# Performance work log

Hardware: AMD Instinct MI355X
Metric: run time of the kernel (lower is better)

Reference implementation:

```python
import jax, jax.numpy as jnp
import numpy as np

# dims
B, N, D = 256, 77, 768     # batch, CLIP tokens, token dim
K, Dn, H = 16, 768, 8      # nodes, node dim, heads
HID, L = 512, 2            # edge-MLP hidden, num GNN layers


def setup_inputs() -> dict:
    key = jax.random.key(0)
    ks = jax.random.split(key, 12)
    g = lambda k, shape, s=0.02: (jax.random.normal(k, shape, jnp.float32) * s)
    return {
        "w": jax.random.normal(ks[0], (B, N, D), jnp.float32),
        "token_mask": jax.random.randint(ks[1], (B, N), 0, 2).astype(jnp.int32),
        "node_queries": g(ks[2], (1, K, Dn)),
        "Wq": g(ks[3], (Dn, Dn)), "bq": jnp.zeros((Dn,), jnp.float32),
        "Wk": g(ks[4], (D, Dn)),  "bk": jnp.zeros((Dn,), jnp.float32),
        "Wv": g(ks[5], (D, Dn)),  "bv": jnp.zeros((Dn,), jnp.float32),
        "We1": g(ks[6], (2 * Dn, HID)), "be1": jnp.zeros((HID,), jnp.float32),
        "We2": g(ks[7], (HID, 1)),      "be2": jnp.zeros((1,), jnp.float32),
        "fuse_gate": jnp.float32(0.0),
        "Wg": g(ks[8], (L, Dn, Dn)), "bg": jnp.zeros((L, Dn), jnp.float32),
    }


def _edge_logits(V, We1, be1, We2, be2):
    # edge_mlp(cat[Vi, Vj]) without materializing [B,K,K,2Dn]:
    # split first linear into the Vi-half and Vj-half of its weight.
    hi = V @ We1[:Dn]   # [B,K,HID]
    hj = V @ We1[Dn:]   # [B,K,HID]
    h = jax.nn.relu(hi[:, :, None, :] + hj[:, None, :, :] + be1)  # [B,K,K,HID]
    return jnp.einsum('bijh,h->bij', h, We2[:, 0]) + be2[0]       # [B,K,K]


def _forward(w, node_queries, Wq, bq, Wk, bk, Wv, bv,
             We1, be1, We2, be2, fuse_gate, Wg, bg, token_mask):
    q = jnp.broadcast_to(node_queries, (B, K, Dn))
    Q = q @ Wq + bq        # [B,K,Dn]
    Kt = w @ Wk + bk       # [B,N,Dn]
    Vt = w @ Wv + bv       # [B,N,Dn]
    # per-head dot products summed over heads == full Dn dot product
    scale = (Dn // H) ** -0.5
    scores = jnp.einsum('bkd,bnd->bkn', Q, Kt) * scale  # [B,K,N]
    pad = (token_mask == 0)[:, None, :]                 # [B,1,N]
    scores = jnp.where(pad, jnp.finfo(scores.dtype).min, scores)
    # softmax over K per token (transpose to [B,N,K])
    S = jax.nn.softmax(jnp.swapaxes(scores, 1, 2), axis=-1)  # [B,N,K]
    V = jnp.einsum('bnk,bnd->bkd', S, Vt)                    # [B,K,Dn]
    gate = jax.nn.sigmoid(fuse_gate)
    V = (1.0 - gate) * V + gate * q
    # pre-GNN edge logits, then relational GNN refinement
    E = _edge_logits(V, We1, be1, We2, be2)
    A = jax.nn.softmax(E, axis=-1)  # [B,K,K], fixed across layers
    for l in range(L):
        msg = jnp.einsum('bij,bjd->bid', A, V @ Wg[l] + bg[l])
        V = V + jax.nn.relu(msg)
    # post-GNN edge logits
    E = _edge_logits(V, We1, be1, We2, be2)
    return S, V, E


def reference(w, token_mask, node_queries, Wq, bq, Wk, bk, Wv, bv,
              We1, be1, We2, be2, fuse_gate, Wg, bg):
    return _forward(w, node_queries, Wq, bq, Wk, bk, Wv, bv,
                    We1, be1, We2, be2, fuse_gate, Wg, bg, token_mask)
```

## Files before the change

kernel.cpp:

```cpp
#include <hip/hip_runtime.h>

typedef unsigned short u16;
typedef __attribute__((ext_vector_type(8))) short short8;
typedef __attribute__((ext_vector_type(4))) float f32x4;

#define DEV static __device__ __forceinline__

DEV float bf2f(u16 u) { return __uint_as_float(((unsigned)u) << 16); }
DEV u16 f2bf(float f) {
  unsigned u = __float_as_uint(f);
  return (u16)((u + 0x7fffu + ((u >> 16) & 1u)) >> 16);
}

DEV void cp16(void* lds, const void* g) {
  __builtin_amdgcn_global_load_lds(
      (const __attribute__((address_space(1))) unsigned int*)g,
      (__attribute__((address_space(3))) unsigned int*)lds, 16, 0, 0);
}

DEV int xcd_swz() {
  int bid = blockIdx.x;
  int cpx = gridDim.x >> 3;
  return (bid & 7) * cpx + (bid >> 3);
}


__global__ __launch_bounds__(256) void tcast_all(const float* __restrict__ Wv,
                                                 const float* __restrict__ We1,
                                                 const float* __restrict__ Wg,
                                                 u16* __restrict__ WvT,
                                                 u16* __restrict__ We1T,
                                                 u16* __restrict__ WgT) {
  __shared__ float tile[32][33];
  const float* src; u16* dst; int C;
  switch (blockIdx.z) {
    case 0: src = Wv;           dst = WvT;           C = 768; break;
    case 1: src = We1;          dst = We1T;          C = 512; break;
    case 2: src = We1 + 393216; dst = We1T + 393216; C = 512; break;
    case 3: src = Wg;           dst = WgT;           C = 768; break;
    default: src = Wg + 589824; dst = WgT + 589824;  C = 768; break;
  }
  int r0 = blockIdx.y * 32, c0 = blockIdx.x * 32;
  if (c0 >= C) return;
  int tr = threadIdx.x >> 5, tc = threadIdx.x & 31;
#pragma unroll
  for (int rr = 0; rr < 4; ++rr)
    tile[tr + rr * 8][tc] = src[(size_t)(r0 + tr + rr * 8) * C + c0 + tc];
  __syncthreads();
#pragma unroll
  for (int rr = 0; rr < 4; ++rr)
    dst[(size_t)(c0 + tr + rr * 8) * 768 + r0 + tc] = f2bf(tile[tc][tr + rr * 8]);
}

__global__ __launch_bounds__(256) void q_part(const float* __restrict__ nq,
                                              const float* __restrict__ Wq,
                                              float* __restrict__ Qpart) {
  int gid = blockIdx.x * 256 + threadIdx.x;
  int s = blockIdx.y;
  int k = gid / 768, d = gid % 768;
  const float* nr = nq + k * 768 + s * 96;
  const float* wp = Wq + (size_t)(s * 96) * 768 + d;
  float s0 = 0.f, s1 = 0.f, s2 = 0.f, s3 = 0.f;
#pragma unroll
  for (int c = 0; c < 96; c += 4) {
    s0 += nr[c + 0] * wp[(size_t)(c + 0) * 768];
    s1 += nr[c + 1] * wp[(size_t)(c + 1) * 768];
    s2 += nr[c + 2] * wp[(size_t)(c + 2) * 768];
    s3 += nr[c + 3] * wp[(size_t)(c + 3) * 768];
  }
  Qpart[(size_t)s * 12288 + gid] = (s0 + s1) + (s2 + s3);
}

__global__ __launch_bounds__(256) void q_reduce(const float* __restrict__ Qpart,
                                                const float* __restrict__ bq,
                                                float* __restrict__ Qf) {
  int gid = blockIdx.x * 256 + threadIdx.x;
  int d = gid % 768;
  float s = bq[d];
#pragma unroll
  for (int i = 0; i < 8; ++i) s += Qpart[(size_t)i * 12288 + gid];
  Qf[gid] = s;
}

__global__ __launch_bounds__(256) void pt_kernel(const float* __restrict__ Qf,
                                                 const float* __restrict__ Wk,
                                                 const float* __restrict__ bk,
                                                 u16* __restrict__ PT16,
                                                 float* __restrict__ qb) {
  int t = threadIdx.x;
  if (blockIdx.x == 48) {
    int k = t >> 4, j = t & 15;
    const float* q = Qf + k * 768 + j * 48;
    const float* bp = bk + j * 48;
    float s = 0.f;
#pragma unroll
    for (int d = 0; d < 48; d += 4) {
      f32x4 qv = *(const f32x4*)&q[d];
      f32x4 bv4 = *(const f32x4*)&bp[d];
      s += qv[0] * bv4[0] + qv[1] * bv4[1] + qv[2] * bv4[2] + qv[3] * bv4[3];
    }
#pragma unroll
    for (int off = 1; off < 16; off <<= 1) s += __shfl_xor(s, off);
    if (j == 0) qb[k] = s;
    return;
  }
  int gid = blockIdx.x * 256 + t;
  int c = gid >> 4, k = gid & 15;
  const float* wr = Wk + (size_t)c * 768;
  const float* q = Qf + k * 768;
  float s = 0.f;
  for (int d = 0; d < 768; d += 4) {
    f32x4 wv = *(const f32x4*)&wr[d];
    f32x4 qv = *(const f32x4*)&q[d];
    s += wv[0] * qv[0] + wv[1] * qv[1] + wv[2] * qv[2] + wv[3] * qv[3];
  }
  PT16[k * 768 + c] = f2bf(s);
}

__global__ __launch_bounds__(256) void score2(const float* __restrict__ w,
                                              const u16* __restrict__ PT16,
                                              const float* __restrict__ qb,
                                              const int* __restrict__ mask,
                                              float* __restrict__ Sout) {
  __shared__ u16 Ps[16 * 776];
  int t = threadIdx.x, wave = t >> 6, lane = t & 63, l16 = lane & 15, quad = lane >> 4;
  int m0 = blockIdx.x * 64;
#pragma unroll
  for (int r = 0; r < 6; ++r) {
    int idx = t + 256 * r;
    int row = idx / 96, c8 = idx % 96;
    *(short8*)&Ps[row * 776 + c8 * 8] = *(const short8*)&PT16[row * 768 + c8 * 8];
  }
  __syncthreads();
  int row = m0 + wave * 16 + l16;
  const float* ap = w + (size_t)row * 768 + quad * 8;
  f32x4 acc = {0.f, 0.f, 0.f, 0.f};
#pragma unroll
  for (int it = 0; it < 24; ++it) {
    f32x4 a0 = *(const f32x4*)(ap + it * 32);
    f32x4 a1 = *(const f32x4*)(ap + it * 32 + 4);
    short8 fa;
#pragma unroll
    for (int e = 0; e < 4; ++e) { fa[e] = (short)f2bf(a0[e]); fa[e + 4] = (short)f2bf(a1[e]); }
    short8 fb = *(const short8*)&Ps[l16 * 776 + it * 32 + quad * 8];
    acc = __builtin_amdgcn_mfma_f32_16x16x32_bf16(fa, fb, acc, 0, 0, 0);
  }
  float qv = qb[l16];
  const float scale = 0.1020620726159658f;
#pragma unroll
  for (int r = 0; r < 4; ++r) {
    int orow = m0 + wave * 16 + quad * 4 + r;
    float s = (acc[r] + qv) * scale;
    if (mask[orow] == 0) s = -3.402823466e38f;
    float mx = s;
#pragma unroll
    for (int off = 1; off < 16; off <<= 1) mx = fmaxf(mx, __shfl_xor(mx, off));
    float e = __expf(s - mx);
    float sm = e;
#pragma unroll
    for (int off = 1; off < 16; off <<= 1) sm += __shfl_xor(sm, off);
    Sout[(size_t)orow * 16 + l16] = e / sm;
  }
}

__global__ __launch_bounds__(256) void u_kernel(const float* __restrict__ Sg,
                                                const float* __restrict__ w,
                                                u16* __restrict__ U16,
                                                float* __restrict__ sk) {
  __shared__ float Ss[1232];
  int b = blockIdx.x, t = threadIdx.x;
  int d = blockIdx.y * 256 + t;
#pragma unroll
  for (int r = 0; r < 5; ++r) {
    int idx = t + 256 * r;
    if (idx < 1232) Ss[idx] = Sg[(size_t)b * 1232 + idx];
  }
  __syncthreads();
  float a[16];
#pragma unroll
  for (int k = 0; k < 16; ++k) a[k] = 0.f;
  const float* wp = w + (size_t)b * 59136;
  for (int n = 0; n < 77; ++n) {
    float g = wp[(size_t)n * 768 + d];
    const float* sr = &Ss[n * 16];
#pragma unroll
    for (int k = 0; k < 16; ++k) a[k] += sr[k] * g;
  }
#pragma unroll
  for (int k = 0; k < 16; ++k)
    U16[(size_t)b * 12288 + (size_t)k * 768 + d] = f2bf(a[k]);
  if (blockIdx.y == 0 && t < 16) {
    float s = 0.f;
    for (int n = 0; n < 77; ++n) s += Ss[n * 16 + t];
    sk[b * 16 + t] = s;
  }
}

#define STAGE3(KOFF, BI)                          \
  do {                                            \
    cp16(AsW + (BI) * 2048, Ap + (KOFF));         \
    cp16(BsW1 + (BI) * 4096, Bp1 + (KOFF));       \
    cp16(BsW2 + (BI) * 4096, Bp2 + (KOFF));       \
  } while (0)

__global__ __launch_bounds__(256) void vgemm(const u16* __restrict__ A,
                                             const u16* __restrict__ BT,
                                             const float* __restrict__ skp,
                                             const float* __restrict__ bv,
                                             const float* __restrict__ nq,
                                             const float* __restrict__ gatep,
                                             float* __restrict__ V32,
                                             u16* __restrict__ V16) {
  __shared__ u16 As[3 * 64 * 32];
  __shared__ u16 Bs[3 * 128 * 32];
  int swz = xcd_swz();
  int mi = swz / 6, ni = swz % 6;
  int m0 = mi * 64, n0 = ni * 128;
  int t = threadIdx.x;
  int wave = t >> 6, lane = t & 63, l16 = lane & 15, quad = lane >> 4;
  int ra = wave * 16 + (lane >> 2);
  int rb1 = wave * 32 + (lane >> 2);
  int rb2 = rb1 + 16;
  int cslot = lane & 3;
  int cga = (cslot ^ ((ra >> 1) & 3)) * 8;
  int cgb1 = (cslot ^ ((rb1 >> 1) & 3)) * 8;
  int cgb2 = (cslot ^ ((rb2 >> 1) & 3)) * 8;

  const u16* Ap = A + (size_t)(m0 + ra) * 768 + cga;
  const u16* Bp1 = BT + (size_t)(n0 + rb1) * 768 + cgb1;
  const u16* Bp2 = BT + (size_t)(n0 + rb2) * 768 + cgb2;
  u16* AsW = &As[(wave * 16) * 32];
  u16* BsW1 = &Bs[(wave * 32) * 32];
  u16* BsW2 = &Bs[(wave * 32 + 16) * 32];

  f32x4 zero4 = {0.f, 0.f, 0.f, 0.f};
  f32x4 acc[4][2];
#pragma unroll
  for (int i = 0; i < 4; ++i) { acc[i][0] = zero4; acc[i][1] = zero4; }

  STAGE3(0, 0); STAGE3(32, 1); STAGE3(64, 2);

  int bi = 0;
  for (int k0 = 0; k0 < 768; k0 += 32) {
    int rem = (768 - 32 - k0) >> 5;
    if (rem >= 2)      asm volatile("s_waitcnt vmcnt(6)" ::: "memory");
    else if (rem == 1) asm volatile("s_waitcnt vmcnt(3)" ::: "memory");
    else               asm volatile("s_waitcnt vmcnt(0)" ::: "memory");
    asm volatile("s_barrier" ::: "memory");
    const u16* Ab = &As[bi * 2048];
    const u16* Bb = &Bs[bi * 4096];
    short8 fa[4], fb[2];
#pragma unroll
    for (int i = 0; i < 4; ++i) {
      int R = i * 16 + l16;
      fa[i] = *(const short8*)&Ab[R * 32 + (quad ^ ((R >> 1) & 3)) * 8];
    }
#pragma unroll
    for (int j = 0; j < 2; ++j) {
      int R = wave * 32 + j * 16 + l16;
      fb[j] = *(const short8*)&Bb[R * 32 + (quad ^ ((R >> 1) & 3)) * 8];
    }
#pragma unroll
    for (int i = 0; i < 4; ++i)
#pragma unroll
      for (int j = 0; j < 2; ++j)
        acc[i][j] = __builtin_amdgcn_mfma_f32_16x16x32_bf16(fa[i], fb[j], acc[i][j], 0, 0, 0);
    asm volatile("s_barrier" ::: "memory");
    if (k0 + 96 < 768) STAGE3(k0 + 96, bi);
    bi = bi + 1; if (bi == 3) bi = 0;
  }

  float gv = gatep[0];
  float g = 1.f / (1.f + __expf(-gv)), og = 1.f - g;
  int narr[2]; float bvj[2];
#pragma unroll
  for (int j = 0; j < 2; ++j) {
    narr[j] = n0 + wave * 32 + j * 16 + l16;
    bvj[j] = bv[narr[j]];
  }
#pragma unroll
  for (int i = 0; i < 4; ++i)
#pragma unroll
    for (int r = 0; r < 4; ++r) {
      int m = m0 + i * 16 + quad * 4 + r;
      float skv = skp[m];
      size_t mrow = (size_t)m * 768;
      const float* nqr = nq + (m & 15) * 768;
#pragma unroll
      for (int j = 0; j < 2; ++j) {
        float val = acc[i][j][r] + skv * bvj[j];
        float v = og * val + g * nqr[narr[j]];
        V32[mrow + narr[j]] = v;
        V16[mrow + narr[j]] = f2bf(v);
      }
    }
}

__global__ __launch_bounds__(256) void gemm16s(const u16* __restrict__ A,
                                               const u16* __restrict__ BT0,
                                               const float* __restrict__ bias0,
                                               u16* __restrict__ C0, int N0, int ntA,
                                               const u16* __restrict__ BT1,
                                               const float* __restrict__ bias1,
                                               u16* __restrict__ C1, int N1, int ntB,
                                               int K) {
  __shared__ u16 As[3 * 64 * 32];
  __shared__ u16 Bs[3 * 128 * 32];
  int nt = ntA + ntB;
  int swz = xcd_swz();
  int mi = swz / nt, ni = swz % nt;
  const u16* BT; const float* bias; u16* C; int N, n0;
  if (ni < ntA) { BT = BT0; bias = bias0; C = C0; N = N0; n0 = ni * 128; }
  else          { BT = BT1; bias = bias1; C = C1; N = N1; n0 = (ni - ntA) * 128; }
  int m0 = mi * 64;
  int t = threadIdx.x;
  int wave = t >> 6, lane = t & 63, l16 = lane & 15, quad = lane >> 4;
  int ra = wave * 16 + (lane >> 2);
  int rb1 = wave * 32 + (lane >> 2);
  int rb2 = rb1 + 16;
  int cslot = lane & 3;
  int cga = (cslot ^ ((ra >> 1) & 3)) * 8;
  int cgb1 = (cslot ^ ((rb1 >> 1) & 3)) * 8;
  int cgb2 = (cslot ^ ((rb2 >> 1) & 3)) * 8;

  const u16* Ap = A + (size_t)(m0 + ra) * K + cga;
  const u16* Bp1 = BT + (size_t)(n0 + rb1) * K + cgb1;
  const u16* Bp2 = BT + (size_t)(n0 + rb2) * K + cgb2;
  u16* AsW = &As[(wave * 16) * 32];
  u16* BsW1 = &Bs[(wave * 32) * 32];
  u16* BsW2 = &Bs[(wave * 32 + 16) * 32];

  f32x4 zero4 = {0.f, 0.f, 0.f, 0.f};
  f32x4 acc[4][2];
#pragma unroll
  for (int i = 0; i < 4; ++i) { acc[i][0] = zero4; acc[i][1] = zero4; }

  STAGE3(0, 0); STAGE3(32, 1); STAGE3(64, 2);

  int bi = 0;
  for (int k0 = 0; k0 < K; k0 += 32) {
    int rem = (K - 32 - k0) >> 5;
    if (rem >= 2)      asm volatile("s_waitcnt vmcnt(6)" ::: "memory");
    else if (rem == 1) asm volatile("s_waitcnt vmcnt(3)" ::: "memory");
    else               asm volatile("s_waitcnt vmcnt(0)" ::: "memory");
    asm volatile("s_barrier" ::: "memory");
    const u16* Ab = &As[bi * 2048];
    const u16* Bb = &Bs[bi * 4096];
    short8 fa[4], fb[2];
#pragma unroll
    for (int i = 0; i < 4; ++i) {
      int R = i * 16 + l16;
      fa[i] = *(const short8*)&Ab[R * 32 + (quad ^ ((R >> 1) & 3)) * 8];
    }
#pragma unroll
    for (int j = 0; j < 2; ++j) {
      int R = wave * 32 + j * 16 + l16;
      fb[j] = *(const short8*)&Bb[R * 32 + (quad ^ ((R >> 1) & 3)) * 8];
    }
#pragma unroll
    for (int i = 0; i < 4; ++i)
#pragma unroll
      for (int j = 0; j < 2; ++j)
        acc[i][j] = __builtin_amdgcn_mfma_f32_16x16x32_bf16(fa[i], fb[j], acc[i][j], 0, 0, 0);
    asm volatile("s_barrier" ::: "memory");
    if (k0 + 96 < K) STAGE3(k0 + 96, bi);
    bi = bi + 1; if (bi == 3) bi = 0;
  }

  int narr[2]; float bvj[2];
#pragma unroll
  for (int j = 0; j < 2; ++j) {
    narr[j] = n0 + wave * 32 + j * 16 + l16;
    bvj[j] = bias ? bias[narr[j]] : 0.f;
  }
#pragma unroll
  for (int i = 0; i < 4; ++i)
#pragma unroll
    for (int r = 0; r < 4; ++r) {
      size_t mrow = (size_t)(m0 + i * 16 + quad * 4 + r) * N;
#pragma unroll
      for (int j = 0; j < 2; ++j)
        C[mrow + narr[j]] = f2bf(acc[i][j][r] + bvj[j]);
    }
}

__global__ __launch_bounds__(256) void edge_kernel(const u16* __restrict__ HIJ,
                                                   const float* __restrict__ be1,
                                                   const float* __restrict__ We2,
                                                   const float* __restrict__ be2v,
                                                   float* __restrict__ Aout,
                                                   float* __restrict__ Eout) {
  __shared__ float hiS[8 * 516];
  __shared__ float hjS[16 * 516];
  __shared__ float be1s[512];
  __shared__ float w2s[512];
  int b = blockIdx.x, ih = blockIdx.y, t = threadIdx.x;
  be1s[t] = be1[t]; be1s[t + 256] = be1[t + 256];
  w2s[t] = We2[t];  w2s[t + 256] = We2[t + 256];

#pragma unroll
  for (int r = 0; r < 6; ++r) {
    int idx = t + 256 * r;
    const u16* src;
    float* dst;
    if (idx < 512) {
      int row = idx >> 6, c8 = idx & 63;
      src = &HIJ[(size_t)(b * 16 + ih * 8 + row) * 1024 + c8 * 8];
      dst = &hiS[row * 516 + c8 * 8];
    } else {
      int k = idx - 512;
      int row = k >> 6, c8 = k & 63;
      src = &HIJ[(size_t)(b * 16 + row) * 1024 + 512 + c8 * 8];
      dst = &hjS[row * 516 + c8 * 8];
    }
    short8 hv = *(const short8*)src;
    f32x4 l0, l1;
#pragma unroll
    for (int ee = 0; ee < 4; ++ee) { l0[ee] = bf2f((u16)hv[ee]); l1[ee] = bf2f((u16)hv[ee + 4]); }
    *(f32x4*)dst = l0;
    *(f32x4*)(dst + 4) = l1;
  }
  __syncthreads();

  int i_loc = t >> 5, j = (t >> 1) & 15, hh = t & 1;
  const float* hi = &hiS[i_loc * 516 + hh * 256];
  const float* hj = &hjS[j * 516 + hh * 256];
  const float* b1 = &be1s[hh * 256];
  const float* w2 = &w2s[hh * 256];
  float e = 0.f;
#pragma unroll 2
  for (int h4 = 0; h4 < 64; ++h4) {
    f32x4 hv = *(const f32x4*)&hi[h4 * 4];
    f32x4 jv = *(const f32x4*)&hj[h4 * 4];
    f32x4 bv = *(const f32x4*)&b1[h4 * 4];
    f32x4 wv = *(const f32x4*)&w2[h4 * 4];
#pragma unroll
    for (int ee = 0; ee < 4; ++ee)
      e += fmaxf(hv[ee] + jv[ee] + bv[ee], 0.f) * wv[ee];
  }
  e += __shfl_xor(e, 1);
  e += be2v[0];

  int pair = (ih * 8 + i_loc) * 16 + j;
  if (Aout) {
    float mx = e;
#pragma unroll
    for (int off = 2; off < 32; off <<= 1) mx = fmaxf(mx, __shfl_xor(mx, off));
    float ex = __expf(e - mx);
    float sm = ex;
#pragma unroll
    for (int off = 2; off < 32; off <<= 1) sm += __shfl_xor(sm, off);
    if (hh == 0) Aout[(size_t)b * 256 + pair] = ex / sm;
  }
  if (Eout && hh == 0) Eout[(size_t)b * 256 + pair] = e;
}

__global__ __launch_bounds__(256) void combine_kernel(const float* __restrict__ Aws,
                                                      const u16* __restrict__ G,
                                                      float* __restrict__ V32,
                                                      u16* __restrict__ V16,
                                                      float* __restrict__ Vout) {
  __shared__ float Gs[16 * 260];
  __shared__ float As[256];
  int b = blockIdx.x, yc = blockIdx.y, t = threadIdx.x;
#pragma unroll
  for (int r = 0; r < 2; ++r) {
    int idx = t + 256 * r;
    int row = idx >> 5, c8 = idx & 31;
    short8 gv8 = *(const short8*)&G[(size_t)(b * 16 + row) * 768 + yc * 256 + c8 * 8];
    f32x4 l0, l1;
#pragma unroll
    for (int ee = 0; ee < 4; ++ee) { l0[ee] = bf2f((u16)gv8[ee]); l1[ee] = bf2f((u16)gv8[ee + 4]); }
    *(f32x4*)&Gs[row * 260 + c8 * 8] = l0;
    *(f32x4*)&Gs[row * 260 + c8 * 8 + 4] = l1;
  }
  As[t] = Aws[(size_t)b * 256 + t];
  __syncthreads();
  int d = yc * 256 + t;
  float gv[16];
#pragma unroll
  for (int j = 0; j < 16; ++j) gv[j] = Gs[j * 260 + t];
#pragma unroll
  for (int i = 0; i < 16; ++i) {
    float msg = 0.f;
#pragma unroll
    for (int j = 0; j < 16; ++j) msg += As[i * 16 + j] * gv[j];
    size_t idx = (size_t)b * 12288 + (size_t)i * 768 + d;
    float v = V32[idx] + fmaxf(msg, 0.f);
    V32[idx] = v;
    V16[idx] = f2bf(v);
    if (Vout) Vout[idx] = v;
  }
}

extern "C" void kernel_launch(void* const* d_in, const int* in_sizes, int n_in,
                              void* d_out, int out_size, void* d_ws, size_t ws_size,
                              hipStream_t stream) {
  const float* w    = (const float*)d_in[0];
  const int*   mask = (const int*)d_in[1];
  const float* nq   = (const float*)d_in[2];
  const float* Wq   = (const float*)d_in[3];
  const float* bq   = (const float*)d_in[4];
  const float* Wk   = (const float*)d_in[5];
  const float* bk   = (const float*)d_in[6];
  const float* Wv   = (const float*)d_in[7];
  const float* bv   = (const float*)d_in[8];
  const float* We1  = (const float*)d_in[9];
  const float* be1  = (const float*)d_in[10];
  const float* We2  = (const float*)d_in[11];
  const float* be2  = (const float*)d_in[12];
  const float* gate = (const float*)d_in[13];
  const float* Wg   = (const float*)d_in[14];
  const float* bg   = (const float*)d_in[15];

  float* ws    = (float*)d_ws;
  float* V32   = ws;
  float* Aws   = V32 + 3145728;
  float* Qpart = Aws + 65536;
  float* Qf    = Qpart + 98304;
  float* qb    = Qf + 12288;
  float* sk    = qb + 16;
  u16* PT16    = (u16*)(sk + 4096);
  u16* WvT     = PT16 + 12288;
  u16* We1T    = WvT + 589824;
  u16* WgT     = We1T + 786432;
  u16* V16     = WgT + 1179648;
  u16* U16     = V16 + 3145728;
  u16* HIJ     = U16 + 3145728;
  u16* Gws     = HIJ + 4194304;

  float* out  = (float*)d_out;
  float* Sout = out;
  float* Vout = out + 315392;
  float* Eout = out + 315392 + 3145728;

  dim3 blk(256);

  tcast_all<<<dim3(24, 24, 5), blk, 0, stream>>>(Wv, We1, Wg, WvT, We1T, WgT);
  q_part<<<dim3(48, 8), blk, 0, stream>>>(nq, Wq, Qpart);
  q_reduce<<<48, blk, 0, stream>>>(Qpart, bq, Qf);
  pt_kernel<<<49, blk, 0, stream>>>(Qf, Wk, bk, PT16, qb);

  score2<<<308, blk, 0, stream>>>(w, PT16, qb, mask, Sout);

  u_kernel<<<dim3(256, 3), blk, 0, stream>>>(Sout, w, U16, sk);
  vgemm<<<384, blk, 0, stream>>>(U16, WvT, sk, bv, nq, gate, V32, V16);

  gemm16s<<<896, blk, 0, stream>>>(V16, We1T, nullptr, HIJ, 1024, 8,
                                   WgT, bg, Gws, 768, 6, 768);
  edge_kernel<<<dim3(256, 2), blk, 0, stream>>>(HIJ, be1, We2, be2, Aws, (float*)nullptr);
  combine_kernel<<<dim3(256, 3), blk, 0, stream>>>(Aws, Gws, V32, V16, (float*)nullptr);

  gemm16s<<<384, blk, 0, stream>>>(V16, WgT + 589824, bg + 768, Gws, 768, 6,
                                   WgT + 589824, bg + 768, Gws, 768, 0, 768);
  combine_kernel<<<dim3(256, 3), blk, 0, stream>>>(Aws, Gws, V32, V16, Vout);

  gemm16s<<<512, blk, 0, stream>>>(V16, We1T, nullptr, HIJ, 1024, 8,
                                   We1T, nullptr, HIJ, 1024, 0, 768);
  edge_kernel<<<dim3(256, 2), blk, 0, stream>>>(HIJ, be1, We2, be2, (float*)nullptr, Eout);
}
```

Measured before the change: 302.3 us.

## Add 128x128 bf16 MFMA GEMM, merge Q kernels, skip redundant V32 store

Adds a gemm128 kernel that uses 128x128 output tiles, double-buffered LDS fed by global_load_lds, and 16x16x32 bf16 MFMA. It replaces the first fused We1/Wg GEMM launch (448 blocks instead of 896), raising operand reuse per block at the cost of fewer blocks per CU. It also merges the split-K q_part/q_reduce pair into one kernel, which drops a launch but lengthens the serial K loop. In the final combine it writes only Vout rather than both V32 and Vout, removing a redundant store.

After: 316.2 us. 4.6% more time.

```diff
diff --git a/kernel.cpp b/kernel.cpp
--- a/kernel.cpp
+++ b/kernel.cpp
@@ -52,34 +52,23 @@
     dst[(size_t)(c0 + tr + rr * 8) * 768 + r0 + tc] = f2bf(tile[tc][tr + rr * 8]);
 }
 
-__global__ __launch_bounds__(256) void q_part(const float* __restrict__ nq,
-                                              const float* __restrict__ Wq,
-                                              float* __restrict__ Qpart) {
+__global__ __launch_bounds__(256) void q_kernel(const float* __restrict__ nq,
+                                                const float* __restrict__ Wq,
+                                                const float* __restrict__ bq,
+                                                float* __restrict__ Qf) {
   int gid = blockIdx.x * 256 + threadIdx.x;
-  int s = blockIdx.y;
   int k = gid / 768, d = gid % 768;
-  const float* nr = nq + k * 768 + s * 96;
-  const float* wp = Wq + (size_t)(s * 96) * 768 + d;
+  const float* nr = nq + k * 768;
+  const float* wp = Wq + d;
   float s0 = 0.f, s1 = 0.f, s2 = 0.f, s3 = 0.f;
-#pragma unroll
-  for (int c = 0; c < 96; c += 4) {
+#pragma unroll 4
+  for (int c = 0; c < 768; c += 4) {
     s0 += nr[c + 0] * wp[(size_t)(c + 0) * 768];
     s1 += nr[c + 1] * wp[(size_t)(c + 1) * 768];
     s2 += nr[c + 2] * wp[(size_t)(c + 2) * 768];
     s3 += nr[c + 3] * wp[(size_t)(c + 3) * 768];
   }
-  Qpart[(size_t)s * 12288 + gid] = (s0 + s1) + (s2 + s3);
-}
-
-__global__ __launch_bounds__(256) void q_reduce(const float* __restrict__ Qpart,
-                                                const float* __restrict__ bq,
-                                                float* __restrict__ Qf) {
-  int gid = blockIdx.x * 256 + threadIdx.x;
-  int d = gid % 768;
-  float s = bq[d];
-#pragma unroll
-  for (int i = 0; i < 8; ++i) s += Qpart[(size_t)i * 12288 + gid];
-  Qf[gid] = s;
+  Qf[gid] = (s0 + s1) + (s2 + s3) + bq[d];
 }
 
 __global__ __launch_bounds__(256) void pt_kernel(const float* __restrict__ Qf,
@@ -384,6 +373,99 @@
     }
 }
 
+#define STG128(BI, KOFF)                                    \
+  do {                                                      \
+    cp16(&As[(BI) * 4096 + (wave * 32) * 32],      Ap1 + (KOFF)); \
+    cp16(&As[(BI) * 4096 + (wave * 32 + 16) * 32], Ap2 + (KOFF)); \
+    cp16(&Bs[(BI) * 4096 + (wave * 32) * 32],      Bp1 + (KOFF)); \
+    cp16(&Bs[(BI) * 4096 + (wave * 32 + 16) * 32], Bp2 + (KOFF)); \
+  } while (0)
+
+__global__ __launch_bounds__(256) void gemm128(const u16* __restrict__ A,
+                                               const u16* __restrict__ BT0,
+                                               const float* __restrict__ bias0,
+                                               u16* __restrict__ C0, int N0, int ntA,
+                                               const u16* __restrict__ BT1,
+                                               const float* __restrict__ bias1,
+                                               u16* __restrict__ C1, int N1, int ntB,
+                                               int K) {
+  __shared__ u16 As[2 * 128 * 32];
+  __shared__ u16 Bs[2 * 128 * 32];
+  int nt = ntA + ntB;
+  int swz = xcd_swz();
+  int mi = swz / nt, ni = swz % nt;
+  const u16* BT; const float* bias; u16* C; int N, n0;
+  if (ni < ntA) { BT = BT0; bias = bias0; C = C0; N = N0; n0 = ni * 128; }
+  else          { BT = BT1; bias = bias1; C = C1; N = N1; n0 = (ni - ntA) * 128; }
+  int m0 = mi * 128;
+  int t = threadIdx.x;
+  int wave = t >> 6, lane = t & 63, l16 = lane & 15, quad = lane >> 4;
+  int wrow = (wave >> 1) * 64, wcol = (wave & 1) * 64;
+  int r1 = wave * 32 + (lane >> 2);
+  int r2 = r1 + 16;
+  int cslot = lane & 3;
+  int cg1 = (cslot ^ ((r1 >> 1) & 3)) * 8;
+  int cg2 = (cslot ^ ((r2 >> 1) & 3)) * 8;
+
+  const u16* Ap1 = A + (size_t)(m0 + r1) * K + cg1;
+  const u16* Ap2 = A + (size_t)(m0 + r2) * K + cg2;
+  const u16* Bp1 = BT + (size_t)(n0 + r1) * K + cg1;
+  const u16* Bp2 = BT + (size_t)(n0 + r2) * K + cg2;
+
+  f32x4 zero4 = {0.f, 0.f, 0.f, 0.f};
+  f32x4 acc[4][4];
+#pragma unroll
+  for (int i = 0; i < 4; ++i)
+#pragma unroll
+    for (int j = 0; j < 4; ++j) acc[i][j] = zero4;
+
+  STG128(0, 0); STG128(1, 32);
+
+  int cur = 0;
+  for (int k0 = 0; k0 < K; k0 += 32) {
+    if (k0 + 32 < K) asm volatile("s_waitcnt vmcnt(4)" ::: "memory");
+    else             asm volatile("s_waitcnt vmcnt(0)" ::: "memory");
+    asm volatile("s_barrier" ::: "memory");
+    const u16* Ab = &As[cur * 4096];
+    const u16* Bb = &Bs[cur * 4096];
+    short8 fa[4], fb[4];
+#pragma unroll
+    for (int i = 0; i < 4; ++i) {
+      int R = wrow + i * 16 + l16;
+      fa[i] = *(const short8*)&Ab[R * 32 + (quad ^ ((R >> 1) & 3)) * 8];
+    }
+#pragma unroll
+    for (int j = 0; j < 4; ++j) {
+      int R = wcol + j * 16 + l16;
+      fb[j] = *(const short8*)&Bb[R * 32 + (quad ^ ((R >> 1) & 3)) * 8];
+    }
+#pragma unroll
+    for (int i = 0; i < 4; ++i)
+#pragma unroll
+      for (int j = 0; j < 4; ++j)
+        acc[i][j] = __builtin_amdgcn_mfma_f32_16x16x32_bf16(fa[i], fb[j], acc[i][j], 0, 0, 0);
+    asm volatile("s_barrier" ::: "memory");
+    if (k0 + 64 < K) STG128(cur, k0 + 64);
+    cur ^= 1;
+  }
+
+  int narr[4]; float bvj[4];
+#pragma unroll
+  for (int j = 0; j < 4; ++j) {
+    narr[j] = n0 + wcol + j * 16 + l16;
+    bvj[j] = bias ? bias[narr[j]] : 0.f;
+  }
+#pragma unroll
+  for (int i = 0; i < 4; ++i)
+#pragma unroll
+    for (int r = 0; r < 4; ++r) {
+      size_t mrow = (size_t)(m0 + wrow + i * 16 + quad * 4 + r) * N;
+#pragma unroll
+      for (int j = 0; j < 4; ++j)
+        C[mrow + narr[j]] = f2bf(acc[i][j][r] + bvj[j]);
+    }
+}
+
 __global__ __launch_bounds__(256) void edge_kernel(const u16* __restrict__ HIJ,
                                                    const float* __restrict__ be1,
                                                    const float* __restrict__ We2,
@@ -487,9 +569,9 @@
     for (int j = 0; j < 16; ++j) msg += As[i * 16 + j] * gv[j];
     size_t idx = (size_t)b * 12288 + (size_t)i * 768 + d;
     float v = V32[idx] + fmaxf(msg, 0.f);
-    V32[idx] = v;
+    if (Vout) { Vout[idx] = v; }
+    else      { V32[idx] = v; }
     V16[idx] = f2bf(v);
-    if (Vout) Vout[idx] = v;
   }
 }
 
@@ -516,8 +598,7 @@
   float* ws    = (float*)d_ws;
   float* V32   = ws;
   float* Aws   = V32 + 3145728;
-  float* Qpart = Aws + 65536;
-  float* Qf    = Qpart + 98304;
+  float* Qf    = Aws + 65536;
   float* qb    = Qf + 12288;
   float* sk    = qb + 16;
   u16* PT16    = (u16*)(sk + 4096);
@@ -537,8 +618,7 @@
   dim3 blk(256);
 
   tcast_all<<<dim3(24, 24, 5), blk, 0, stream>>>(Wv, We1, Wg, WvT, We1T, WgT);
-  q_part<<<dim3(48, 8), blk, 0, stream>>>(nq, Wq, Qpart);
-  q_reduce<<<48, blk, 0, stream>>>(Qpart, bq, Qf);
+  q_kernel<<<48, blk, 0, stream>>>(nq, Wq, bq, Qf);
   pt_kernel<<<49, blk, 0, stream>>>(Qf, Wk, bk, PT16, qb);
 
   score2<<<308, blk, 0, stream>>>(w, PT16, qb, mask, Sout);
@@ -546,7 +626,7 @@
   u_kernel<<<dim3(256, 3), blk, 0, stream>>>(Sout, w, U16, sk);
   vgemm<<<384, blk, 0, stream>>>(U16, WvT, sk, bv, nq, gate, V32, V16);
 
-  gemm16s<<<896, blk, 0, stream>>>(V16, We1T, nullptr, HIJ, 1024, 8,
+  gemm128<<<448, blk, 0, stream>>>(V16, We1T, nullptr, HIJ, 1024, 8,
                                    WgT, bg, Gws, 768, 6, 768);
   edge_kernel<<<dim3(256, 2), blk, 0, stream>>>(HIJ, be1, We2, be2, Aws, (float*)nullptr);
   combine_kernel<<<dim3(256, 3), blk, 0, stream>>>(Aws, Gws, V32, V16, (float*)nullptr);
```
